# Kernel optimization log

Hardware: AMD Instinct MI355X
Metric: run time of the kernel (lower is better)

## Reference

```python
import jax, jax.numpy as jnp
import numpy as np

WINDOW_LENGTH = 512
ORDER = 26


def hann_window(n):
    # periodic Hann (matches torch.hann_window default)
    i = jnp.arange(n, dtype=jnp.float32)
    return 0.5 * (1.0 - jnp.cos(2.0 * jnp.pi * i / n))


def upsample_linear(g, hop):
    # F.interpolate(mode='linear', align_corners=False), scale_factor=hop
    B, F = g.shape
    j = jnp.arange(F * hop, dtype=jnp.float32)
    src = jnp.clip((j + 0.5) / hop - 0.5, 0.0, F - 1.0)
    i0 = jnp.floor(src).astype(jnp.int32)
    i1 = jnp.minimum(i0 + 1, F - 1)
    w = src - i0.astype(jnp.float32)
    return g[:, i0] * (1.0 - w) + g[:, i1] * w


def lpc_synthesis_batch(x, a):
    # all-pole IIR: y[n] = x[n] - sum_k a[k] * y[n-1-k]; x [N,W], a [N,order]
    N, W = x.shape
    order = a.shape[1]

    def step(carry, xt):  # carry [N,order] newest-first, xt [N]
        yt = xt - jnp.sum(a * carry, axis=1)
        carry = jnp.concatenate([yt[:, None], carry[:, :-1]], axis=1)
        return carry, yt

    _, y = jax.lax.scan(step, jnp.zeros((N, order), x.dtype), x.T)
    return y.T  # [N, W]


def setup_inputs() -> dict:
    key = jax.random.key(0)
    k1, k2, k3 = jax.random.split(key, 3)
    B, T, F = 32, 128000, 1000
    ex = jax.random.normal(k1, (B, T), dtype=jnp.float32)
    gain = jax.random.uniform(k2, (B, F), dtype=jnp.float32)
    # small coefficients keep the all-pole filter stable
    a = jax.random.normal(k3, (B, F, ORDER), dtype=jnp.float32) * 0.05
    window = hann_window(WINDOW_LENGTH)
    return {"ex": ex, "gain": gain, "a": a, "window": window, "hop_length": 128}


def reference(ex, gain, a, window, hop_length):
    W = window.shape[0]
    pad = (W - hop_length) // 2
    B = ex.shape[0]
    ug = upsample_linear(gain, hop_length)  # [B, F*hop]
    T = min(ex.shape[1], ug.shape[1])
    exg = ex[:, :T] * ug[:, :T]
    exp = jnp.pad(exg, ((0, 0), (pad, pad)))
    nframes = (exp.shape[1] - W) // hop_length + 1
    idx = jnp.arange(nframes)[:, None] * hop_length + jnp.arange(W)[None, :]  # [F,W]
    unfolded = exp[:, idx]  # [B, F, W]
    a_ = a[:, :nframes].reshape(-1, a.shape[-1])
    filt = lpc_synthesis_batch(unfolded.reshape(-1, W), a_).reshape(B, nframes, W)
    windowed = filt * window  # window applied per in-frame sample (diag kernel)
    L = (nframes - 1) * hop_length + W
    flat_idx = idx.reshape(-1)
    ola = jnp.zeros((B, L), filt.dtype).at[:, flat_idx].add(windowed.reshape(B, -1))
    norm = jnp.zeros((L,), filt.dtype).at[flat_idx].add(jnp.tile(window, nframes))
    return ola[:, pad:L - pad] / norm[pad:L - pad]
```

## Files before the change

### kernel.cpp

```cpp
#include <hip/hip_runtime.h>
#include <hip/hip_bf16.h>

#define BATCH   32
#define TLEN    128000
#define FGAIN   1000
#define ORDER   26
#define WLEN    512
#define HOP     128
#define PAD     192
#define TPAD    (TLEN + 2*PAD)
#define NFRAME  1000
#define NTOT    (BATCH*NFRAME)

#define CHUNK   64
#define NCHUNK  ((NFRAME + CHUNK - 1) / CHUNK)
#define XS_SPAN (CHUNK*HOP + WLEN - HOP)
#define XS_LDS  8656
#define GS_LDS  80
#define YSTRIDE 53

#define WAVE_LDS_FENCE() asm volatile("s_waitcnt lgkmcnt(0)" ::: "memory")

__global__ __launch_bounds__(64) void k_lpc(const float* __restrict__ ex,
                                            const float* __restrict__ gain,
                                            const float* __restrict__ acoef,
                                            float* __restrict__ fw) {
  __shared__ float xs[XS_LDS];
  __shared__ float gs[GS_LDS];
  __shared__ float as_lin[CHUNK * ORDER];
  __shared__ float ys[CHUNK * YSTRIDE];

  const int lane = threadIdx.x;
  const int n0   = blockIdx.x * CHUNK;
  const int b    = blockIdx.y;
  const float* __restrict__ exr = ex + (size_t)b * TLEN;
  const float* __restrict__ gr  = gain + b * FGAIN;

  const int GBASE = n0 - 2;
  for (int i = lane; i < 72; i += 64) {
    int gidx = GBASE + i;
    gidx = gidx < 0 ? 0 : (gidx > FGAIN - 1 ? FGAIN - 1 : gidx);
    gs[i] = gr[gidx];
  }
  __syncthreads();

  {
    const int e0_4 = (b * NFRAME + n0) * ORDER / 4;
    const int lim4 = NTOT * ORDER / 4;
    for (int v = lane; v < CHUNK * ORDER / 4; v += 64) {
      float4 c = make_float4(0.f, 0.f, 0.f, 0.f);
      if (e0_4 + v < lim4)
        c = *reinterpret_cast<const float4*>(acoef + 4 * (size_t)(e0_4 + v));
      *reinterpret_cast<float4*>(as_lin + 4 * v) = c;
    }
  }

  const int sbase = n0 * HOP;
#define STAGE_COMPUTE(IDX4, EVAL) {                                        \
    int sc_s = 4 * (IDX4);                                                 \
    int sc_j = sbase + sc_s - PAD;                                         \
    float sc_v[4] = {0.f, 0.f, 0.f, 0.f};                                  \
    if (sc_j >= 0 && sc_j <= TLEN - 4) {                                   \
      float sc_e[4] = {(EVAL).x, (EVAL).y, (EVAL).z, (EVAL).w};            \
      _Pragma("unroll")                                                    \
      for (int sc_c = 0; sc_c < 4; ++sc_c) {                               \
        float sc_src = ((float)(sc_j + sc_c) + 0.5f) * (1.0f / (float)HOP) \
                       - 0.5f;                                             \
        sc_src = fminf(fmaxf(sc_src, 0.0f), (float)(FGAIN - 1));           \
        int   sc_i0 = (int)sc_src;                                         \
        float sc_w  = sc_src - (float)sc_i0;                               \
        int   sc_i1 = sc_i0 + 1; if (sc_i1 > FGAIN - 1) sc_i1 = FGAIN - 1; \
        float sc_g  = gs[sc_i0 - GBASE] * (1.0f - sc_w)                    \
                    + gs[sc_i1 - GBASE] * sc_w;                            \
        sc_v[sc_c] = sc_e[sc_c] * sc_g;                                    \
      }                                                                    \
    }                                                                      \
    int sc_b = sc_s + (sc_s >> 7);              \
    xs[sc_b + 0] = sc_v[0];  xs[sc_b + 1] = sc_v[1];                       \
    xs[sc_b + 2] = sc_v[2];  xs[sc_b + 3] = sc_v[3];                       \
  }
  for (int g8 = 0; g8 < 4; ++g8) {
    float4 ev[8];
#pragma unroll
    for (int u = 0; u < 8; ++u) {
      int gi = lane + 64 * (8 * g8 + u);
      int gj = sbase + 4 * gi - PAD;
      ev[u] = make_float4(0.f, 0.f, 0.f, 0.f);
      if (gj >= 0 && gj <= TLEN - 4)
        ev[u] = *reinterpret_cast<const float4*>(exr + gj);
    }
#pragma unroll
    for (int u = 0; u < 8; ++u) {
      STAGE_COMPUTE(lane + 64 * (8 * g8 + u), ev[u])
    }
  }
  {
    int ti = lane + 2048;
    int tj = sbase + 4 * ti - PAD;
    float4 te = make_float4(0.f, 0.f, 0.f, 0.f);
    if (tj >= 0 && tj <= TLEN - 4)
      te = *reinterpret_cast<const float4*>(exr + tj);
    STAGE_COMPUTE(ti, te)
  }
  if (lane < XS_SPAN / 4 - 2112) {
    int ti = lane + 2112;
    int tj = sbase + 4 * ti - PAD;
    float4 te = make_float4(0.f, 0.f, 0.f, 0.f);
    if (tj >= 0 && tj <= TLEN - 4)
      te = *reinterpret_cast<const float4*>(exr + tj);
    STAGE_COMPUTE(ti, te)
  }
#undef STAGE_COMPUTE
  __syncthreads();

  float a[ORDER], h[ORDER];
  {
    const float* __restrict__ al = as_lin + lane * ORDER;
#pragma unroll
    for (int q = 0; q < 13; ++q) {
      float2 v = *reinterpret_cast<const float2*>(al + 2 * q);
      a[2 * q] = v.x;  a[2 * q + 1] = v.y;
    }
  }
#pragma unroll
  for (int k = 0; k < ORDER; ++k) h[k] = 0.0f;

  const size_t fwrow0 = (size_t)(b * NFRAME + n0) * WLEN;
  float buf[52];

#define LPC_STEP(s) {                                                      \
    float xv = buf[(s)];                                                   \
    float p0 = xv, p1 = 0.f, p2 = 0.f, p3 = 0.f;                           \
    _Pragma("unroll")                                                      \
    for (int k = 1; k < ORDER; ++k) {                                      \
      float hv = h[((s) - 1 - k + 2 * ORDER) % ORDER];                     \
      int sel = k & 3;                                                     \
      if      (sel == 0) p0 -= a[k] * hv;                                  \
      else if (sel == 1) p1 -= a[k] * hv;                                  \
      else if (sel == 2) p2 -= a[k] * hv;                                  \
      else               p3 -= a[k] * hv;                                  \
    }                                                                      \
    float rest = (p0 + p1) + (p2 + p3);                                    \
    float y = rest - a[0] * h[((s) + ORDER - 1) % ORDER];                  \
    h[(s) % ORDER] = y;                                                    \
    ys[lane * YSTRIDE + (s)] = y;                                          \
  }

#define LOAD_BUF(nq) {                                                     \
    _Pragma("unroll")                                                      \
    for (int q = 0; q < (nq); ++q) {                                       \
      int u = t + 4 * q;                                                   \
      int base = lane * 129 + u + (u >> 7);                                \
      buf[4 * q + 0] = xs[base + 0];                                       \
      buf[4 * q + 1] = xs[base + 1];                                       \
      buf[4 * q + 2] = xs[base + 2];                                       \
      buf[4 * q + 3] = xs[base + 3];                                       \
    }                                                                      \
  }

#define STORE_YS(nq) {                                                     \
    WAVE_LDS_FENCE();          \
    _Pragma("unroll")                                                      \
    for (int jj = 0; jj < 4; ++jj) {                                       \
      int q = (lane & 3) + 4 * jj;                                         \
      if (q < (nq)) {                                                      \
        _Pragma("unroll")                                                  \
        for (int rr = 0; rr < 4; ++rr) {                                   \
          int r = rr * 16 + (lane >> 2);                                   \
          if ((n0 + r) < NFRAME) {                                         \
            float4 vv = make_float4(ys[r * YSTRIDE + 4 * q + 0],           \
                                    ys[r * YSTRIDE + 4 * q + 1],           \
                                    ys[r * YSTRIDE + 4 * q + 2],           \
                                    ys[r * YSTRIDE + 4 * q + 3]);          \
            *reinterpret_cast<float4*>(fw + fwrow0 + (size_t)r * WLEN      \
                                       + t + 4 * q) = vv;                  \
          }                                                                \
        }                                                                  \
      }                                                                    \
    }                                                                      \
    WAVE_LDS_FENCE();           \
  }

  int t = 0;
  for (int sb = 0; sb < 9; ++sb) {
    LOAD_BUF(13)
#pragma unroll
    for (int s = 0; s < 52; ++s) {
      LPC_STEP(s)
    }
    STORE_YS(13)
    t += 52;
  }
  LOAD_BUF(11)
#pragma unroll
  for (int s = 0; s < 44; ++s) {
    LPC_STEP(s)
  }
  STORE_YS(11)
#undef LPC_STEP
#undef LOAD_BUF
#undef STORE_YS
}

__global__ __launch_bounds__(256) void k_ola(const float* __restrict__ fw,
                                             const float* __restrict__ win,
                                             float* __restrict__ out) {
  int gid = blockIdx.x * 256 + threadIdx.x;
  const int total4 = BATCH * TLEN / 4;
  if (gid >= total4) return;
  int idx = gid * 4;
  int b  = idx / TLEN;
  int j0 = idx - b * TLEN;
  int p0 = j0 + PAD;

  int lo = (p0 - 381) / HOP;
  if (lo < 0) lo = 0;
  int hi = p0 / HOP;
  if (hi > NFRAME - 1) hi = NFRAME - 1;

  float ax = 0.f, ay = 0.f, az = 0.f, aw = 0.f;
  float nx = 0.f, ny = 0.f, nz = 0.f, nw = 0.f;
  for (int n = lo; n <= hi; ++n) {
    int w0 = p0 - n * HOP;
    const float4 fv = *reinterpret_cast<const float4*>(fw + ((size_t)b * NFRAME + n) * WLEN + w0);
    const float4 wv = *reinterpret_cast<const float4*>(win + w0);
    ax += fv.x * wv.x;  ay += fv.y * wv.y;  az += fv.z * wv.z;  aw += fv.w * wv.w;
    nx += wv.x;         ny += wv.y;         nz += wv.z;         nw += wv.w;
  }
  float4 o = make_float4(ax / nx, ay / ny, az / nz, aw / nw);
  *reinterpret_cast<float4*>(out + idx) = o;
}

extern "C" void kernel_launch(void* const* d_in, const int* in_sizes, int n_in,
                              void* d_out, int out_size, void* d_ws, size_t ws_size,
                              hipStream_t stream) {
  const float* ex   = (const float*)d_in[0];
  const float* gain = (const float*)d_in[1];
  const float* a    = (const float*)d_in[2];
  const float* win  = (const float*)d_in[3];
  float* outp = (float*)d_out;

  float* fw = (float*)d_ws;

  {
    hipLaunchKernelGGL(k_lpc, dim3(NCHUNK, BATCH), dim3(64), 0, stream,
                       ex, gain, a, fw);
  }
  {
    int total4 = BATCH * TLEN / 4;
    int blocks = (total4 + 255) / 256;
    hipLaunchKernelGGL(k_ola, dim3(blocks), dim3(256), 0, stream, fw, win, outp);
  }
}
```

Baseline: 127.7 us.

## Store LPC output in frame-interleaved layout directly from registers

The LPC kernel now writes filtered samples straight from registers into a workspace laid out as [batch][chunk][sample/4][frame-in-chunk] float4. This makes each wave's store coalesced without staging through LDS and drops the ys buffer and wait fences. The overlap-add kernel is updated to index this layout, which makes its per-thread reads strided across lanes. It also writes padded frames of the last chunk, enlarging the workspace footprint. The coefficient-loading loop is also unrolled.

Result: no change. 129.4 us (+1.3%).

```diff
diff --git a/kernel.cpp b/kernel.cpp
--- a/kernel.cpp
+++ b/kernel.cpp
@@ -6,6 +6,7 @@
 #define FGAIN   1000
 #define ORDER   26
 #define WLEN    512
+#define WLEN4   (WLEN/4)
 #define HOP     128
 #define PAD     192
 #define TPAD    (TLEN + 2*PAD)
@@ -17,21 +18,19 @@
 #define XS_SPAN (CHUNK*HOP + WLEN - HOP)
 #define XS_LDS  8656
 #define GS_LDS  80
-#define YSTRIDE 53
-
-#define WAVE_LDS_FENCE() asm volatile("s_waitcnt lgkmcnt(0)" ::: "memory")
+
 
 __global__ __launch_bounds__(64) void k_lpc(const float* __restrict__ ex,
                                             const float* __restrict__ gain,
                                             const float* __restrict__ acoef,
-                                            float* __restrict__ fw) {
+                                            float4* __restrict__ fwt) {
   __shared__ float xs[XS_LDS];
   __shared__ float gs[GS_LDS];
   __shared__ float as_lin[CHUNK * ORDER];
-  __shared__ float ys[CHUNK * YSTRIDE];
 
   const int lane = threadIdx.x;
-  const int n0   = blockIdx.x * CHUNK;
+  const int cidx = blockIdx.x;
+  const int n0   = cidx * CHUNK;
   const int b    = blockIdx.y;
   const float* __restrict__ exr = ex + (size_t)b * TLEN;
   const float* __restrict__ gr  = gain + b * FGAIN;
@@ -47,11 +46,15 @@
   {
     const int e0_4 = (b * NFRAME + n0) * ORDER / 4;
     const int lim4 = NTOT * ORDER / 4;
-    for (int v = lane; v < CHUNK * ORDER / 4; v += 64) {
-      float4 c = make_float4(0.f, 0.f, 0.f, 0.f);
-      if (e0_4 + v < lim4)
-        c = *reinterpret_cast<const float4*>(acoef + 4 * (size_t)(e0_4 + v));
-      *reinterpret_cast<float4*>(as_lin + 4 * v) = c;
+#pragma unroll
+    for (int it = 0; it < 7; ++it) {
+      int v = lane + 64 * it;
+      if (v < CHUNK * ORDER / 4) {
+        float4 c = make_float4(0.f, 0.f, 0.f, 0.f);
+        if (e0_4 + v < lim4)
+          c = *reinterpret_cast<const float4*>(acoef + 4 * (size_t)(e0_4 + v));
+        *reinterpret_cast<float4*>(as_lin + 4 * v) = c;
+      }
     }
   }
 
@@ -125,7 +128,7 @@
 #pragma unroll
   for (int k = 0; k < ORDER; ++k) h[k] = 0.0f;
 
-  const size_t fwrow0 = (size_t)(b * NFRAME + n0) * WLEN;
+  float4* __restrict__ fwt_blk = fwt + (size_t)(b * NCHUNK + cidx) * WLEN4 * CHUNK;
   float buf[52];
 
 #define LPC_STEP(s) {                                                      \
@@ -143,7 +146,7 @@
     float rest = (p0 + p1) + (p2 + p3);                                    \
     float y = rest - a[0] * h[((s) + ORDER - 1) % ORDER];                  \
     h[(s) % ORDER] = y;                                                    \
-    ys[lane * YSTRIDE + (s)] = y;                                          \
+    buf[(s)] = y;                                                          \
   }
 
 #define LOAD_BUF(nq) {                                                     \
@@ -158,27 +161,13 @@
     }                                                                      \
   }
 
-#define STORE_YS(nq) {                                                     \
-    WAVE_LDS_FENCE();          \
+#define STORE_BUF(nq) {                                                    \
     _Pragma("unroll")                                                      \
-    for (int jj = 0; jj < 4; ++jj) {                                       \
-      int q = (lane & 3) + 4 * jj;                                         \
-      if (q < (nq)) {                                                      \
-        _Pragma("unroll")                                                  \
-        for (int rr = 0; rr < 4; ++rr) {                                   \
-          int r = rr * 16 + (lane >> 2);                                   \
-          if ((n0 + r) < NFRAME) {                                         \
-            float4 vv = make_float4(ys[r * YSTRIDE + 4 * q + 0],           \
-                                    ys[r * YSTRIDE + 4 * q + 1],           \
-                                    ys[r * YSTRIDE + 4 * q + 2],           \
-                                    ys[r * YSTRIDE + 4 * q + 3]);          \
-            *reinterpret_cast<float4*>(fw + fwrow0 + (size_t)r * WLEN      \
-                                       + t + 4 * q) = vv;                  \
-          }                                                                \
-        }                                                                  \
-      }                                                                    \
-    }                                                                      \
-    WAVE_LDS_FENCE();           \
+    for (int q = 0; q < (nq); ++q) {                                       \
+      fwt_blk[(size_t)((t >> 2) + q) * CHUNK + lane] =                     \
+          make_float4(buf[4 * q + 0], buf[4 * q + 1],                      \
+                      buf[4 * q + 2], buf[4 * q + 3]);                     \
+    }                                                                      \
   }
 
   int t = 0;
@@ -188,7 +177,7 @@
     for (int s = 0; s < 52; ++s) {
       LPC_STEP(s)
     }
-    STORE_YS(13)
+    STORE_BUF(13)
     t += 52;
   }
   LOAD_BUF(11)
@@ -196,13 +185,13 @@
   for (int s = 0; s < 44; ++s) {
     LPC_STEP(s)
   }
-  STORE_YS(11)
+  STORE_BUF(11)
 #undef LPC_STEP
 #undef LOAD_BUF
-#undef STORE_YS
+#undef STORE_BUF
 }
 
-__global__ __launch_bounds__(256) void k_ola(const float* __restrict__ fw,
+__global__ __launch_bounds__(256) void k_ola(const float4* __restrict__ fwt,
                                              const float* __restrict__ win,
                                              float* __restrict__ out) {
   int gid = blockIdx.x * 256 + threadIdx.x;
@@ -218,11 +207,12 @@
   int hi = p0 / HOP;
   if (hi > NFRAME - 1) hi = NFRAME - 1;
 
+  const size_t brow = (size_t)b * NCHUNK * WLEN4 * CHUNK;
   float ax = 0.f, ay = 0.f, az = 0.f, aw = 0.f;
   float nx = 0.f, ny = 0.f, nz = 0.f, nw = 0.f;
   for (int n = lo; n <= hi; ++n) {
     int w0 = p0 - n * HOP;
-    const float4 fv = *reinterpret_cast<const float4*>(fw + ((size_t)b * NFRAME + n) * WLEN + w0);
+    float4 fv = fwt[brow + ((size_t)(n >> 6) * WLEN4 + (w0 >> 2)) * CHUNK + (n & 63)];
     const float4 wv = *reinterpret_cast<const float4*>(win + w0);
     ax += fv.x * wv.x;  ay += fv.y * wv.y;  az += fv.z * wv.z;  aw += fv.w * wv.w;
     nx += wv.x;         ny += wv.y;         nz += wv.z;         nw += wv.w;
@@ -240,15 +230,15 @@
   const float* win  = (const float*)d_in[3];
   float* outp = (float*)d_out;
 
-  float* fw = (float*)d_ws;
+  float4* fwt = (float4*)d_ws;
 
   {
     hipLaunchKernelGGL(k_lpc, dim3(NCHUNK, BATCH), dim3(64), 0, stream,
-                       ex, gain, a, fw);
+                       ex, gain, a, fwt);
   }
   {
     int total4 = BATCH * TLEN / 4;
     int blocks = (total4 + 255) / 256;
-    hipLaunchKernelGGL(k_ola, dim3(blocks), dim3(256), 0, stream, fw, win, outp);
+    hipLaunchKernelGGL(k_ola, dim3(blocks), dim3(256), 0, stream, fwt, win, outp);
   }
 }
```
